# Kernel optimization log

Hardware: AMD Instinct MI355X
Metric: run time of the kernel (lower is better)

Reference implementation:

```python
import jax, jax.numpy as jnp
import numpy as np

N_PTS = 10000
BATCH = 2048          # hypotheses per RANSAC iteration
MAX_ITER = 10
SAMPLE_SIZE = 4       # minimal sample for homography DLT
INL_TH = 2.0          # squared symmetric transfer error threshold
EPS = 1e-8


def normalize_points(pts):
    # kornia.geometry.normalize_points: center + isotropic scale to mean dist sqrt(2)
    mean = pts.mean(axis=1, keepdims=True)                       # [B,1,2]
    d = jnp.linalg.norm(pts - mean, axis=-1).mean(axis=-1)       # [B]
    s = jnp.sqrt(jnp.asarray(2.0, pts.dtype)) / (d + EPS)
    B = pts.shape[0]
    T = jnp.zeros((B, 3, 3), pts.dtype)
    T = T.at[:, 0, 0].set(s).at[:, 1, 1].set(s).at[:, 2, 2].set(1.0)
    T = T.at[:, 0, 2].set(-s * mean[:, 0, 0]).at[:, 1, 2].set(-s * mean[:, 0, 1])
    return (pts - mean) * s[:, None, None], T


def find_homography_dlt(p1, p2):
    # p1,p2: [B,4,2]; weights are all ones -> solve smallest eigvec of A^T A (as kornia does)
    p1n, T1 = normalize_points(p1)
    p2n, T2 = normalize_points(p2)
    x1, y1 = p1n[..., 0], p1n[..., 1]
    x2, y2 = p2n[..., 0], p2n[..., 1]
    o = jnp.ones_like(x1); z = jnp.zeros_like(x1)
    ax = jnp.stack([z, z, z, -x1, -y1, -o, y2 * x1, y2 * y1, y2], -1)
    ay = jnp.stack([x1, y1, o, z, z, z, -x2 * x1, -x2 * y1, -x2], -1)
    A = jnp.concatenate([ax, ay], axis=1)                        # [B,8,9]
    AtA = jnp.einsum('bki,bkj->bij', A, A)                       # [B,9,9]
    _, _, Vh = jnp.linalg.svd(AtA)
    H = Vh[:, -1, :].reshape(-1, 3, 3)                           # smallest singular vector
    H = jnp.linalg.inv(T2) @ (H @ T1)
    return H / (H[:, 2:3, 2:3] + EPS)


def transform_points(H, pts):
    # H: [B,3,3], pts: [N,2] -> [B,N,2] (safe homogeneous division, as kornia)
    ph = jnp.concatenate([pts, jnp.ones_like(pts[..., :1])], -1)  # [N,3]
    pt = jnp.einsum('bij,nj->bni', H, ph)                        # [B,N,3]
    zc = pt[..., 2:3]
    mask = jnp.abs(zc) > EPS
    scale = jnp.where(mask, 1.0 / jnp.where(mask, zc, jnp.ones_like(zc)), jnp.ones_like(zc))
    return pt[..., :2] * scale


def symmetric_transfer_error(p1, p2, H):
    # squared symmetric transfer error (kornia default squared=True)
    Hinv = jnp.linalg.inv(H)
    e1 = ((transform_points(H, p1) - p2[None]) ** 2).sum(-1)
    e2 = ((transform_points(Hinv, p2) - p1[None]) ** 2).sum(-1)
    return e1 + e2                                               # [B,N]


def ransac_forward(kp1, kp2, key):
    n = kp1.shape[0]
    keys = jax.random.split(key, MAX_ITER)
    init = (jnp.asarray(1.0, kp1.dtype), jnp.eye(3, dtype=kp1.dtype), jnp.zeros((n,), bool))

    def body(carry, k):
        best_score, best_model, best_inl = carry
        # batched sampling without replacement: top-k of iid uniforms == randperm[:k]
        u = jax.random.uniform(k, (BATCH, n))
        _, idxs = jax.lax.top_k(u, SAMPLE_SIZE)                  # [BATCH,4] distinct
        H = find_homography_dlt(kp1[idxs], kp2[idxs])            # [BATCH,3,3]
        # remove_bad_models: mask instead of filter (jit-friendly)
        valid = jnp.abs(jnp.diagonal(H, axis1=1, axis2=2)).min(-1) > 1e-6
        err = symmetric_transfer_error(kp1, kp2, H)              # [BATCH,N]
        inl = err <= INL_TH
        scores = jnp.where(valid, inl.sum(-1).astype(kp1.dtype), -1.0)
        bi = jnp.argmax(scores)
        better = scores[bi] > best_score
        best_score = jnp.where(better, scores[bi], best_score)
        best_model = jnp.where(better, H[bi], best_model)
        best_inl = jnp.where(better, inl[bi], best_inl)
        return (best_score, best_model, best_inl), None

    (_, best_model, best_inl), _ = jax.lax.scan(body, init, keys)
    return best_model, best_inl


def setup_inputs():
    key = jax.random.key(0)
    k1, k2 = jax.random.split(key)
    kp1 = jax.random.uniform(k1, (N_PTS, 2), jnp.float32) * 100.0
    kp2 = jax.random.uniform(k2, (N_PTS, 2), jnp.float32) * 100.0
    return {"kp1": kp1, "kp2": kp2}


def reference(kp1, kp2):
    return ransac_forward(kp1, kp2, jax.random.key(42))
```

## Files before the change

### kernel.cpp

```cpp
#include <hip/hip_runtime.h>
#include <stdint.h>

#define JAX_PARTITIONABLE 1

#define N_PTS    10000
#define BATCH    2048
#define MAX_ITER 10
#define NMODELS  (BATCH*MAX_ITER)

__device__ __forceinline__ uint32_t rotl32(uint32_t v, int d){ return (v<<d)|(v>>(32-d)); }

__device__ __forceinline__ void threefry_rounds(uint32_t k0, uint32_t k1, uint32_t ks2,
                                                uint32_t &x0, uint32_t &x1){
#define TF_R(r) { x0 += x1; x1 = rotl32(x1,(r)); x1 ^= x0; }
  TF_R(13) TF_R(15) TF_R(26) TF_R(6)
  x0 += k1;  x1 += ks2 + 1u;
  TF_R(17) TF_R(29) TF_R(16) TF_R(24)
  x0 += ks2; x1 += k0 + 2u;
  TF_R(13) TF_R(15) TF_R(26) TF_R(6)
  x0 += k0;  x1 += k1 + 3u;
  TF_R(17) TF_R(29) TF_R(16) TF_R(24)
  x0 += k1;  x1 += ks2 + 4u;
  TF_R(13) TF_R(15) TF_R(26) TF_R(6)
  x0 += ks2; x1 += k0 + 5u;
#undef TF_R
}

__device__ __forceinline__ void threefry2x32(uint32_t k0, uint32_t k1, uint32_t &x0, uint32_t &x1){
  const uint32_t ks2 = k0 ^ k1 ^ 0x1BD11BDAu;
  x0 += k0; x1 += k1;
  threefry_rounds(k0, k1, ks2, x0, x1);
}

__device__ __forceinline__ void top4_insert(unsigned long long a[4], unsigned long long key){
  if (key > a[3]){
    if (key > a[0]){ a[3]=a[2]; a[2]=a[1]; a[1]=a[0]; a[0]=key; }
    else if (key > a[1]){ a[3]=a[2]; a[2]=a[1]; a[1]=key; }
    else if (key > a[2]){ a[3]=a[2]; a[2]=key; }
    else { a[3]=key; }
  }
}

__device__ void block_merge_top4(unsigned long long a[4], unsigned long long* sm, int tid){
  sm[tid*4+0]=a[0]; sm[tid*4+1]=a[1]; sm[tid*4+2]=a[2]; sm[tid*4+3]=a[3];
  __syncthreads();
  for (int s = 128; s >= 1; s >>= 1){
    if (tid < s){
      unsigned long long bv[4];
      bv[0]=sm[(tid+s)*4+0]; bv[1]=sm[(tid+s)*4+1]; bv[2]=sm[(tid+s)*4+2]; bv[3]=sm[(tid+s)*4+3];
      unsigned long long ov[4];
      int pa=0, pb=0;
      #pragma unroll
      for (int k=0;k<4;k++){
        unsigned long long va = (pa<4)?a[pa]:0ull;
        unsigned long long vb = (pb<4)?bv[pb]:0ull;
        bool ta = va >= vb;
        ov[k] = ta ? va : vb;
        pa += ta?1:0; pb += ta?0:1;
      }
      a[0]=ov[0]; a[1]=ov[1]; a[2]=ov[2]; a[3]=ov[3];
      sm[tid*4+0]=a[0]; sm[tid*4+1]=a[1]; sm[tid*4+2]=a[2]; sm[tid*4+3]=a[3];
    }
    __syncthreads();
  }
}

#if JAX_PARTITIONABLE
#define TH_BITS 4267479552u
#define CAND_CAP 1024

__global__ __launch_bounds__(256) void sample_topk(int* __restrict__ idxs){
  const int b = blockIdx.x;
  const int t = blockIdx.y;
  const int tid = threadIdx.x;
  uint32_t k0 = 0u, k1 = (uint32_t)t;
  threefry2x32(0u, 42u, k0, k1);
  const uint32_t ks2 = k0 ^ k1 ^ 0x1BD11BDAu;

  __shared__ unsigned long long cand[CAND_CAP];
  __shared__ unsigned long long sm[256*4];
  __shared__ unsigned int cnt;
  if (tid == 0) cnt = 0u;
  __syncthreads();

  const uint32_t jb = (uint32_t)(b * N_PTS) + k1;
  for (int i = tid; i < N_PTS; i += 256){
    uint32_t x0 = k0, x1 = jb + (uint32_t)i;
    threefry_rounds(k0, k1, ks2, x0, x1);
    uint32_t u = x0 ^ x1;
    if (u >= TH_BITS){
      unsigned long long key = ((unsigned long long)(u >> 9) << 32) | (uint32_t)(~(uint32_t)i);
      unsigned int slot = atomicAdd(&cnt, 1u);
      if (slot < CAND_CAP) cand[slot] = key;
    }
  }
  __syncthreads();
  const unsigned int n = cnt;

  unsigned long long a[4] = {0ull,0ull,0ull,0ull};
  if (n >= 4u && n <= (unsigned int)CAND_CAP){
    for (unsigned int c = tid; c < n; c += 256) top4_insert(a, cand[c]);
  } else {
    for (int i = tid; i < N_PTS; i += 256){
      uint32_t x0 = k0, x1 = jb + (uint32_t)i;
      threefry_rounds(k0, k1, ks2, x0, x1);
      uint32_t u = x0 ^ x1;
      unsigned long long key = ((unsigned long long)(u >> 9) << 32) | (uint32_t)(~(uint32_t)i);
      top4_insert(a, key);
    }
  }
  block_merge_top4(a, sm, tid);
  if (tid == 0){
    int base = ((t*BATCH)+b)*4;
    idxs[base+0] = (int)(~(uint32_t)(a[0] & 0xffffffffull));
    idxs[base+1] = (int)(~(uint32_t)(a[1] & 0xffffffffull));
    idxs[base+2] = (int)(~(uint32_t)(a[2] & 0xffffffffull));
    idxs[base+3] = (int)(~(uint32_t)(a[3] & 0xffffffffull));
  }
}
#else
__global__ __launch_bounds__(256) void sample_topk(int* __restrict__ idxs){
  const int b = blockIdx.x;
  const int t = blockIdx.y;
  const int tid = threadIdx.x;
  uint32_t k0, k1;
  {
    int i0 = 2*t, i1 = 2*t+1;
    uint32_t u0, u1;
    if (i0 < 10){ u0=(uint32_t)i0; u1=(uint32_t)(i0+10); threefry2x32(0u,42u,u0,u1); k0=u0; }
    else        { u0=(uint32_t)(i0-10); u1=(uint32_t)i0; threefry2x32(0u,42u,u0,u1); k0=u1; }
    if (i1 < 10){ u0=(uint32_t)i1; u1=(uint32_t)(i1+10); threefry2x32(0u,42u,u0,u1); k1=u0; }
    else        { u0=(uint32_t)(i1-10); u1=(uint32_t)i1; threefry2x32(0u,42u,u0,u1); k1=u1; }
  }
  const uint32_t half = 10240000u;
  unsigned long long aLo[4] = {0,0,0,0}, aHi[4] = {0,0,0,0};
  const uint32_t jbase = (uint32_t)(b * N_PTS);
  for (int i = tid; i < N_PTS; i += 256){
    uint32_t x0 = jbase + (uint32_t)i, x1 = x0 + half;
    threefry2x32(k0, k1, x0, x1);
    unsigned long long kLo = ((unsigned long long)(x0 >> 9) << 32) | (uint32_t)(~(uint32_t)i);
    unsigned long long kHi = ((unsigned long long)(x1 >> 9) << 32) | (uint32_t)(~(uint32_t)i);
    top4_insert(aLo, kLo);
    top4_insert(aHi, kHi);
  }
  __shared__ unsigned long long sm[256*4];
  block_merge_top4(aLo, sm, tid);
  if (tid == 0){
    int base = ((t*BATCH)+b)*4;
    for (int s=0;s<4;s++) idxs[base+s] = (int)(~(uint32_t)(aLo[s] & 0xffffffffull));
  }
  __syncthreads();
  block_merge_top4(aHi, sm, tid);
  if (tid == 0){
    int base = ((t*BATCH)+(b+1024))*4;
    for (int s=0;s<4;s++) idxs[base+s] = (int)(~(uint32_t)(aHi[s] & 0xffffffffull));
  }
}
#endif

__global__ __launch_bounds__(64) void dlt_kernel(const float* __restrict__ kp1,
                                                 const float* __restrict__ kp2,
                                                 const int* __restrict__ idxs,
                                                 float* __restrict__ Hout,
                                                 float* __restrict__ Hinvout,
                                                 int* __restrict__ validout){
  const int m = blockIdx.x*64 + threadIdx.x;
  __shared__ double As[64][73];
  double* A = &As[threadIdx.x][0];

  double p1x[4],p1y[4],p2x[4],p2y[4];
  #pragma unroll
  for (int s=0;s<4;s++){
    int id = idxs[m*4+s];
    float2 a = ((const float2*)kp1)[id];
    float2 b = ((const float2*)kp2)[id];
    p1x[s]=a.x; p1y[s]=a.y; p2x[s]=b.x; p2y[s]=b.y;
  }
  double mx1=0,my1=0,mx2=0,my2=0;
  #pragma unroll
  for (int s=0;s<4;s++){ mx1+=p1x[s]; my1+=p1y[s]; mx2+=p2x[s]; my2+=p2y[s]; }
  mx1*=0.25; my1*=0.25; mx2*=0.25; my2*=0.25;
  double d1=0,d2=0;
  #pragma unroll
  for (int s=0;s<4;s++){
    d1 += sqrt((p1x[s]-mx1)*(p1x[s]-mx1) + (p1y[s]-my1)*(p1y[s]-my1));
    d2 += sqrt((p2x[s]-mx2)*(p2x[s]-mx2) + (p2y[s]-my2)*(p2y[s]-my2));
  }
  d1*=0.25; d2*=0.25;
  const double s1 = sqrt(2.0)/(d1 + 1e-8);
  const double s2 = sqrt(2.0)/(d2 + 1e-8);
  #pragma unroll
  for (int s=0;s<4;s++){
    double X1=(p1x[s]-mx1)*s1, Y1=(p1y[s]-my1)*s1;
    double X2=(p2x[s]-mx2)*s2, Y2=(p2y[s]-my2)*s2;
    double* ra = A + s*9;
    ra[0]=0.0; ra[1]=0.0; ra[2]=0.0; ra[3]=-X1; ra[4]=-Y1; ra[5]=-1.0;
    ra[6]=Y2*X1; ra[7]=Y2*Y1; ra[8]=Y2;
    double* rb = A + (4+s)*9;
    rb[0]=X1; rb[1]=Y1; rb[2]=1.0; rb[3]=0.0; rb[4]=0.0; rb[5]=0.0;
    rb[6]=-X2*X1; rb[7]=-X2*Y1; rb[8]=-X2;
  }
  for (int k=0;k<8;k++){
    int piv=k; double pv=fabs(A[k*9+k]);
    for (int r=k+1;r<8;r++){ double v=fabs(A[r*9+k]); if (v>pv){pv=v;piv=r;} }
    if (piv!=k){
      for (int c=k;c<9;c++){ double tmp=A[k*9+c]; A[k*9+c]=A[piv*9+c]; A[piv*9+c]=tmp; }
    }
    double invp = 1.0/A[k*9+k];
    for (int r=k+1;r<8;r++){
      double f = A[r*9+k]*invp;
      for (int c=k+1;c<9;c++) A[r*9+c] -= f*A[k*9+c];
      A[r*9+k]=0.0;
    }
  }
  double h[9];
  h[8]=1.0;
  for (int k=7;k>=0;k--){
    double ssum=0.0;
    for (int c=k+1;c<9;c++) ssum += A[k*9+c]*h[c];
    h[k] = -ssum / A[k*9+k];
  }
  {
    double nn=0.0;
    #pragma unroll
    for (int i=0;i<9;i++) nn += h[i]*h[i];
    double inr = 1.0/sqrt(nn);
    #pragma unroll
    for (int i=0;i<9;i++) h[i]*=inr;
  }
  double M[9];
  #pragma unroll
  for (int r=0;r<3;r++){
    double h0=h[r*3+0], h1=h[r*3+1], h2=h[r*3+2];
    M[r*3+0] = h0*s1;
    M[r*3+1] = h1*s1;
    M[r*3+2] = h0*(-s1*mx1) + h1*(-s1*my1) + h2;
  }
  double Hd[9];
  const double is2 = 1.0/s2;
  #pragma unroll
  for (int c=0;c<3;c++){
    Hd[0*3+c] = M[0*3+c]*is2 + mx2*M[2*3+c];
    Hd[1*3+c] = M[1*3+c]*is2 + my2*M[2*3+c];
    Hd[2*3+c] = M[2*3+c];
  }
  const double dn = 1.0/(Hd[8] + 1e-8);
  #pragma unroll
  for (int i=0;i<9;i++) Hd[i]*=dn;
  float Hf[9];
  #pragma unroll
  for (int i=0;i<9;i++){ Hf[i]=(float)Hd[i]; Hout[m*9+i]=Hf[i]; }
  float mind = fminf(fminf(fabsf(Hf[0]),fabsf(Hf[4])),fabsf(Hf[8]));
  validout[m] = (mind > 1e-6f) ? 1 : 0;
  {
    double a=Hd[0],b=Hd[1],c=Hd[2],d=Hd[3],e=Hd[4],f=Hd[5],g=Hd[6],hh=Hd[7],ii=Hd[8];
    double C00= e*ii-f*hh, C01=-(d*ii-f*g), C02= d*hh-e*g;
    double det = a*C00 + b*C01 + c*C02;
    double idet = 1.0/det;
    double inv[9];
    inv[0]=C00*idet;        inv[1]=(c*hh-b*ii)*idet; inv[2]=(b*f-c*e)*idet;
    inv[3]=C01*idet;        inv[4]=(a*ii-c*g)*idet;  inv[5]=(c*d-a*f)*idet;
    inv[6]=C02*idet;        inv[7]=(b*g-a*hh)*idet;  inv[8]=(a*e-b*d)*idet;
    #pragma unroll
    for (int i=0;i<9;i++) Hinvout[m*9+i]=(float)inv[i];
  }
}

__device__ __forceinline__ int inlier_test(float x1,float y1,float x2,float y2,
                                           const float* __restrict__ H,
                                           const float* __restrict__ Hi){
  float px = __fadd_rn(__fadd_rn(__fmul_rn(H[0],x1), __fmul_rn(H[1],y1)), H[2]);
  float py = __fadd_rn(__fadd_rn(__fmul_rn(H[3],x1), __fmul_rn(H[4],y1)), H[5]);
  float pz = __fadd_rn(__fadd_rn(__fmul_rn(H[6],x1), __fmul_rn(H[7],y1)), H[8]);
  float sc = (fabsf(pz) > 1e-8f) ? __fdiv_rn(1.0f, pz) : 1.0f;
  float dx = __fsub_rn(__fmul_rn(px,sc), x2);
  float dy = __fsub_rn(__fmul_rn(py,sc), y2);
  float e1 = __fadd_rn(__fmul_rn(dx,dx), __fmul_rn(dy,dy));
  if (!(e1 <= 2.0f)) return 0;
  float qx = __fadd_rn(__fadd_rn(__fmul_rn(Hi[0],x2), __fmul_rn(Hi[1],y2)), Hi[2]);
  float qy = __fadd_rn(__fadd_rn(__fmul_rn(Hi[3],x2), __fmul_rn(Hi[4],y2)), Hi[5]);
  float qz = __fadd_rn(__fadd_rn(__fmul_rn(Hi[6],x2), __fmul_rn(Hi[7],y2)), Hi[8]);
  float sc2 = (fabsf(qz) > 1e-8f) ? __fdiv_rn(1.0f, qz) : 1.0f;
  float ex = __fsub_rn(__fmul_rn(qx,sc2), x1);
  float ey = __fsub_rn(__fmul_rn(qy,sc2), y1);
  float e2 = __fadd_rn(__fmul_rn(ex,ex), __fmul_rn(ey,ey));
  float err = __fadd_rn(e1, e2);
  return (err <= 2.0f) ? 1 : 0;
}

__global__ __launch_bounds__(256) void score_kernel(const float* __restrict__ kp1,
                                                    const float* __restrict__ kp2,
                                                    const float* __restrict__ Hall,
                                                    const float* __restrict__ Hinvall,
                                                    const int* __restrict__ validall,
                                                    float* __restrict__ scores){
  const int m = blockIdx.x;
  __shared__ float sH[9], sHi[9];
  if (threadIdx.x < 9)       sH[threadIdx.x]     = Hall[m*9+threadIdx.x];
  else if (threadIdx.x < 18) sHi[threadIdx.x-9]  = Hinvall[m*9+threadIdx.x-9];
  __syncthreads();
  int cnt = 0;
  for (int i = threadIdx.x; i < N_PTS; i += 256){
    float2 p1 = ((const float2*)kp1)[i];
    float2 p2 = ((const float2*)kp2)[i];
    cnt += inlier_test(p1.x,p1.y,p2.x,p2.y,sH,sHi);
  }
  __shared__ int red[256];
  red[threadIdx.x]=cnt; __syncthreads();
  for (int s=128;s;s>>=1){ if (threadIdx.x<s) red[threadIdx.x]+=red[threadIdx.x+s]; __syncthreads(); }
  if (threadIdx.x==0) scores[m] = validall[m] ? (float)red[0] : -1.0f;
}

__global__ __launch_bounds__(1024) void select_kernel(const float* __restrict__ scores,
                                                      int* __restrict__ winner){
  __shared__ unsigned long long sm[1024];
  const int tid = threadIdx.x;
  unsigned long long best = 0ull;
  for (int i = tid; i < NMODELS; i += 1024){
    float s = scores[i];
    uint32_t hi = (uint32_t)(int)(s + 2.0f);
    unsigned long long key = ((unsigned long long)hi << 32) | (uint32_t)(~(uint32_t)i);
    if (key > best) best = key;
  }
  sm[tid]=best; __syncthreads();
  for (int s=512;s;s>>=1){ if (tid<s && sm[tid+s]>sm[tid]) sm[tid]=sm[tid+s]; __syncthreads(); }
  if (tid==0){
    unsigned long long k = sm[0];
    winner[0] = (int)(~(uint32_t)(k & 0xffffffffull));
    winner[1] = ((uint32_t)(k >> 32) >= 4u) ? 1 : 0;
  }
}

__global__ __launch_bounds__(256) void finalize_kernel(const float* __restrict__ kp1,
                                                       const float* __restrict__ kp2,
                                                       const float* __restrict__ Hall,
                                                       const float* __restrict__ Hinvall,
                                                       const int* __restrict__ winner,
                                                       float* __restrict__ out){
  __shared__ float sH[9], sHi[9];
  const int w = winner[0];
  const int ok = winner[1];
  if (threadIdx.x < 9){
    float idv = (threadIdx.x % 4 == 0) ? 1.0f : 0.0f;
    sH[threadIdx.x]  = ok ? Hall[w*9+threadIdx.x]    : idv;
    sHi[threadIdx.x] = ok ? Hinvall[w*9+threadIdx.x] : idv;
  }
  __syncthreads();
  if (blockIdx.x==0 && threadIdx.x<9) out[threadIdx.x] = sH[threadIdx.x];
  const int i = blockIdx.x*256 + threadIdx.x;
  if (i < N_PTS){
    float2 p1 = ((const float2*)kp1)[i];
    float2 p2 = ((const float2*)kp2)[i];
    int inl = ok ? inlier_test(p1.x,p1.y,p2.x,p2.y,sH,sHi) : 0;
    out[9+i] = inl ? 1.0f : 0.0f;
  }
}

extern "C" void kernel_launch(void* const* d_in, const int* in_sizes, int n_in,
                              void* d_out, int out_size, void* d_ws, size_t ws_size,
                              hipStream_t stream) {
  (void)in_sizes; (void)n_in; (void)out_size; (void)ws_size;
  const float* kp1 = (const float*)d_in[0];
  const float* kp2 = (const float*)d_in[1];
  float* out = (float*)d_out;
  char* ws = (char*)d_ws;
  int*   idxs    = (int*)  (ws + 0);
  float* Hall    = (float*)(ws + 327680);
  float* Hinvall = (float*)(ws + 1064960);
  int*   validall= (int*)  (ws + 1802240);
  float* scores  = (float*)(ws + 1884160);
  int*   winner  = (int*)  (ws + 1966080);

#if JAX_PARTITIONABLE
  sample_topk<<<dim3(BATCH, MAX_ITER), 256, 0, stream>>>(idxs);
#else
  sample_topk<<<dim3(BATCH/2, MAX_ITER), 256, 0, stream>>>(idxs);
#endif
  dlt_kernel<<<dim3(NMODELS/64), 64, 0, stream>>>(kp1, kp2, idxs, Hall, Hinvall, validall);
  score_kernel<<<dim3(NMODELS), 256, 0, stream>>>(kp1, kp2, Hall, Hinvall, validall, scores);
  select_kernel<<<1, 1024, 0, stream>>>(scores, winner);
  finalize_kernel<<<dim3((N_PTS+255)/256), 256, 0, stream>>>(kp1, kp2, Hall, Hinvall, winner, out);
}
```

Baseline: 886.7 us.

## Score four models per block and interleave threefry streams with alignbit rotates

```diff
diff --git a/kernel.cpp b/kernel.cpp
--- a/kernel.cpp
+++ b/kernel.cpp
@@ -8,11 +8,13 @@
 #define MAX_ITER 10
 #define NMODELS  (BATCH*MAX_ITER)
 
+#define ROTL(v,d) __builtin_amdgcn_alignbit((v),(v),(uint32_t)(32-(d)))
+
 __device__ __forceinline__ uint32_t rotl32(uint32_t v, int d){ return (v<<d)|(v>>(32-d)); }
 
 __device__ __forceinline__ void threefry_rounds(uint32_t k0, uint32_t k1, uint32_t ks2,
                                                 uint32_t &x0, uint32_t &x1){
-#define TF_R(r) { x0 += x1; x1 = rotl32(x1,(r)); x1 ^= x0; }
+#define TF_R(r) { x0 += x1; x1 = ROTL(x1,(r)); x1 ^= x0; }
   TF_R(13) TF_R(15) TF_R(26) TF_R(6)
   x0 += k1;  x1 += ks2 + 1u;
   TF_R(17) TF_R(29) TF_R(16) TF_R(24)
@@ -67,7 +69,7 @@
 
 #if JAX_PARTITIONABLE
 #define TH_BITS 4267479552u
-#define CAND_CAP 1024
+#define CAND_CAP 256
 
 __global__ __launch_bounds__(256) void sample_topk(int* __restrict__ idxs){
   const int b = blockIdx.x;
@@ -84,7 +86,52 @@
   __syncthreads();
 
   const uint32_t jb = (uint32_t)(b * N_PTS) + k1;
-  for (int i = tid; i < N_PTS; i += 256){
+
+  {
+    uint32_t x1b = jb + (uint32_t)tid;
+    for (int iter = 0; iter < 9; ++iter, x1b += 1024u){
+      uint32_t a0=k0, a1=k0, a2=k0, a3=k0;
+      uint32_t b0=x1b, b1=x1b+256u, b2=x1b+512u, b3=x1b+768u;
+#define QR4(r) { a0+=b0; b0=ROTL(b0,r); b0^=a0;  a1+=b1; b1=ROTL(b1,r); b1^=a1; \
+                 a2+=b2; b2=ROTL(b2,r); b2^=a2;  a3+=b3; b3=ROTL(b3,r); b3^=a3; }
+#define INJ4(p,q) { a0+=(p); b0+=(q); a1+=(p); b1+=(q); a2+=(p); b2+=(q); a3+=(p); b3+=(q); }
+      QR4(13) QR4(15) QR4(26) QR4(6)
+      INJ4(k1,  ks2 + 1u)
+      QR4(17) QR4(29) QR4(16) QR4(24)
+      INJ4(ks2, k0 + 2u)
+      QR4(13) QR4(15) QR4(26) QR4(6)
+      INJ4(k0,  k1 + 3u)
+      QR4(17) QR4(29) QR4(16) QR4(24)
+      INJ4(k1,  ks2 + 4u)
+      QR4(13) QR4(15) QR4(26) QR4(6)
+      INJ4(ks2, k0 + 5u)
+#undef QR4
+#undef INJ4
+      const uint32_t u0 = a0^b0, u1 = a1^b1, u2 = a2^b2, u3 = a3^b3;
+      const uint32_t ibase = (uint32_t)(iter*1024 + tid);
+      if (u0 >= TH_BITS){
+        unsigned long long key = ((unsigned long long)(u0 >> 9) << 32) | (uint32_t)(~ibase);
+        unsigned int slot = atomicAdd(&cnt, 1u);
+        if (slot < CAND_CAP) cand[slot] = key;
+      }
+      if (u1 >= TH_BITS){
+        unsigned long long key = ((unsigned long long)(u1 >> 9) << 32) | (uint32_t)(~(ibase+256u));
+        unsigned int slot = atomicAdd(&cnt, 1u);
+        if (slot < CAND_CAP) cand[slot] = key;
+      }
+      if (u2 >= TH_BITS){
+        unsigned long long key = ((unsigned long long)(u2 >> 9) << 32) | (uint32_t)(~(ibase+512u));
+        unsigned int slot = atomicAdd(&cnt, 1u);
+        if (slot < CAND_CAP) cand[slot] = key;
+      }
+      if (u3 >= TH_BITS){
+        unsigned long long key = ((unsigned long long)(u3 >> 9) << 32) | (uint32_t)(~(ibase+768u));
+        unsigned int slot = atomicAdd(&cnt, 1u);
+        if (slot < CAND_CAP) cand[slot] = key;
+      }
+    }
+  }
+  for (int i = 9216 + tid; i < N_PTS; i += 256){
     uint32_t x0 = k0, x1 = jb + (uint32_t)i;
     threefry_rounds(k0, k1, ks2, x0, x1);
     uint32_t u = x0 ^ x1;
@@ -288,27 +335,38 @@
   return (err <= 2.0f) ? 1 : 0;
 }
 
+#define MODELS_PER_BLOCK 4
 __global__ __launch_bounds__(256) void score_kernel(const float* __restrict__ kp1,
                                                     const float* __restrict__ kp2,
                                                     const float* __restrict__ Hall,
                                                     const float* __restrict__ Hinvall,
                                                     const int* __restrict__ validall,
                                                     float* __restrict__ scores){
-  const int m = blockIdx.x;
-  __shared__ float sH[9], sHi[9];
-  if (threadIdx.x < 9)       sH[threadIdx.x]     = Hall[m*9+threadIdx.x];
-  else if (threadIdx.x < 18) sHi[threadIdx.x-9]  = Hinvall[m*9+threadIdx.x-9];
-  __syncthreads();
-  int cnt = 0;
-  for (int i = threadIdx.x; i < N_PTS; i += 256){
+  const int m0 = blockIdx.x * MODELS_PER_BLOCK;
+  const int tid = threadIdx.x;
+  __shared__ float sH[MODELS_PER_BLOCK][9], sHi[MODELS_PER_BLOCK][9];
+  if (tid < 9*MODELS_PER_BLOCK)        sH [tid/9][tid%9] = Hall[m0*9 + tid];
+  else if (tid < 18*MODELS_PER_BLOCK){ int q = tid - 9*MODELS_PER_BLOCK;
+                                       sHi[q/9][q%9] = Hinvall[m0*9 + q]; }
+  __syncthreads();
+  int cnt[MODELS_PER_BLOCK];
+  #pragma unroll
+  for (int mm=0;mm<MODELS_PER_BLOCK;mm++) cnt[mm]=0;
+  for (int i = tid; i < N_PTS; i += 256){
     float2 p1 = ((const float2*)kp1)[i];
     float2 p2 = ((const float2*)kp2)[i];
-    cnt += inlier_test(p1.x,p1.y,p2.x,p2.y,sH,sHi);
+    #pragma unroll
+    for (int mm=0;mm<MODELS_PER_BLOCK;mm++)
+      cnt[mm] += inlier_test(p1.x,p1.y,p2.x,p2.y,sH[mm],sHi[mm]);
   }
   __shared__ int red[256];
-  red[threadIdx.x]=cnt; __syncthreads();
-  for (int s=128;s;s>>=1){ if (threadIdx.x<s) red[threadIdx.x]+=red[threadIdx.x+s]; __syncthreads(); }
-  if (threadIdx.x==0) scores[m] = validall[m] ? (float)red[0] : -1.0f;
+  #pragma unroll
+  for (int mm=0;mm<MODELS_PER_BLOCK;mm++){
+    red[tid]=cnt[mm]; __syncthreads();
+    for (int s=128;s;s>>=1){ if (tid<s) red[tid]+=red[tid+s]; __syncthreads(); }
+    if (tid==0) scores[m0+mm] = validall[m0+mm] ? (float)red[0] : -1.0f;
+    __syncthreads();
+  }
 }
 
 __global__ __launch_bounds__(1024) void select_kernel(const float* __restrict__ scores,
@@ -377,7 +435,7 @@
   sample_topk<<<dim3(BATCH/2, MAX_ITER), 256, 0, stream>>>(idxs);
 #endif
   dlt_kernel<<<dim3(NMODELS/64), 64, 0, stream>>>(kp1, kp2, idxs, Hall, Hinvall, validall);
-  score_kernel<<<dim3(NMODELS), 256, 0, stream>>>(kp1, kp2, Hall, Hinvall, validall, scores);
+  score_kernel<<<dim3(NMODELS/MODELS_PER_BLOCK), 256, 0, stream>>>(kp1, kp2, Hall, Hinvall, validall, scores);
   select_kernel<<<1, 1024, 0, stream>>>(scores, winner);
   finalize_kernel<<<dim3((N_PTS+255)/256), 256, 0, stream>>>(kp1, kp2, Hall, Hinvall, winner, out);
 }
```

Result: faster. 749.4 us (-15.5%).
